# Kernel tuning notes

Hardware: AMD Instinct MI355X
Metric: run time of the kernel (lower is better)

## Reference

```python
import jax, jax.numpy as jnp
import numpy as np

N_CFG = 400_000    # total basic-block nodes across the batch
E_CFG = 1_600_000  # CFG edges
N_FUNC = 8_000     # internal functions across the batch
N_EXT = 1_600      # external functions across the batch
N_FCG = N_FUNC + N_EXT
E_FCG = 80_000     # call-graph edges
B = 8              # binaries per batch
D_IN, D_H = 64, 128
VOCAB = 10_002     # max_vocab_size + 2


def gcn_layer(x, edge_index, W, b, n_nodes):
    # PyG GCNConv with self-loops: x' = D^{-1/2}(A+I)D^{-1/2} (x W) + b
    h = x @ W
    row, col = edge_index[0], edge_index[1]
    deg = jax.ops.segment_sum(jnp.ones_like(col, dtype=h.dtype), col, num_segments=n_nodes) + 1.0
    dis = jax.lax.rsqrt(deg)
    norm = (dis[row] * dis[col])[:, None]
    agg = jax.ops.segment_sum(h[row] * norm, col, num_segments=n_nodes)
    return agg + h * (dis * dis)[:, None] + b  # second term is the self-loop message


def segment_mean(x, seg, n):
    s = jax.ops.segment_sum(x, seg, num_segments=n)
    c = jax.ops.segment_sum(jnp.ones((x.shape[0],), x.dtype), seg, num_segments=n)
    return s / jnp.maximum(c, 1.0)[:, None]


def setup_inputs() -> dict:
    key = jax.random.key(0)
    ks = jax.random.split(key, 24)
    s = 0.05
    cfg_x = jax.random.normal(ks[0], (N_CFG, D_IN), jnp.float32)
    cfg_edge_index = jax.random.randint(ks[1], (2, E_CFG), 0, N_CFG)
    cfg_node2func = jnp.sort(jax.random.randint(ks[2], (N_CFG,), 0, N_FUNC))
    fcg_edge_index = jax.random.randint(ks[3], (2, E_FCG), 0, N_FCG)
    fcg_batch = jnp.sort(jax.random.randint(ks[4], (N_FCG,), 0, B))
    # first N_FUNC FCG nodes are internal (index into pooled CFG embeddings),
    # the rest are external (index into the embedding table, avoiding pad idx 0)
    fcg_src_idx = jnp.concatenate([jnp.arange(N_FUNC, dtype=jnp.int64 if jax.config.jax_enable_x64 else jnp.int32).astype(jnp.int32),
                                   jax.random.randint(ks[5], (N_EXT,), 1, VOCAB)])
    fcg_is_ext = jnp.concatenate([jnp.zeros((N_FUNC,), jnp.int32), jnp.ones((N_EXT,), jnp.int32)])
    emb_table = jax.random.normal(ks[6], (VOCAB, D_H), jnp.float32) * s
    emb_table = emb_table.at[0].set(0.0)  # padding_idx row
    return {
        'cfg_x': cfg_x, 'cfg_edge_index': cfg_edge_index, 'cfg_node2func': cfg_node2func,
        'fcg_edge_index': fcg_edge_index, 'fcg_batch': fcg_batch,
        'fcg_src_idx': fcg_src_idx, 'fcg_is_ext': fcg_is_ext,
        'W_cfg1': jax.random.normal(ks[7], (D_IN, D_H), jnp.float32) * s,
        'b_cfg1': jax.random.normal(ks[8], (D_H,), jnp.float32) * s,
        'W_cfg2': jax.random.normal(ks[9], (D_H, D_H), jnp.float32) * s,
        'b_cfg2': jax.random.normal(ks[10], (D_H,), jnp.float32) * s,
        'emb_table': emb_table,
        'W_fcg1': jax.random.normal(ks[11], (D_H, D_H), jnp.float32) * s,
        'b_fcg1': jax.random.normal(ks[12], (D_H,), jnp.float32) * s,
        'Wp1': jax.random.normal(ks[13], (D_H, D_H // 2), jnp.float32) * s,
        'bp1': jax.random.normal(ks[14], (D_H // 2,), jnp.float32) * s,
        'Wp2': jax.random.normal(ks[15], (D_H // 2, D_H // 4), jnp.float32) * s,
        'bp2': jax.random.normal(ks[16], (D_H // 4,), jnp.float32) * s,
        'Wp3': jax.random.normal(ks[17], (D_H // 4, 1), jnp.float32) * s,
        'bp3': jax.random.normal(ks[18], (1,), jnp.float32) * s,
    }


def reference(cfg_x, cfg_edge_index, cfg_node2func, fcg_edge_index, fcg_batch,
              fcg_src_idx, fcg_is_ext, W_cfg1, b_cfg1, W_cfg2, b_cfg2, emb_table,
              W_fcg1, b_fcg1, Wp1, bp1, Wp2, bp2, Wp3, bp3):
    # CFG-level GCN stack (dropout is identity in eval)
    x = jax.nn.relu(gcn_layer(cfg_x, cfg_edge_index, W_cfg1, b_cfg1, N_CFG))
    x = jax.nn.relu(gcn_layer(x, cfg_edge_index, W_cfg2, b_cfg2, N_CFG))
    # global_mean_pool per function
    x_cfg_pool = segment_mean(x, cfg_node2func, N_FUNC)  # [N_FUNC, D_H]
    # assemble FCG node features: internal = pooled CFG embedding, external = embedding lookup
    internal = jnp.take(x_cfg_pool, jnp.clip(fcg_src_idx, 0, N_FUNC - 1), axis=0)
    external = jnp.take(emb_table, fcg_src_idx, axis=0, mode='clip')
    fcg_x = jnp.where((fcg_is_ext == 1)[:, None], external, internal)  # [N_FCG, D_H]
    # FCG-level GCN
    y = jax.nn.relu(gcn_layer(fcg_x, fcg_edge_index, W_fcg1, b_fcg1, N_FCG))
    # global_mean_pool per binary
    g = segment_mean(y, fcg_batch, B)  # [B, D_H]
    # projection head + sigmoid
    h = jax.nn.relu(g @ Wp1 + bp1)
    h = jax.nn.relu(h @ Wp2 + bp2)
    return jax.nn.sigmoid(h @ Wp3 + bp3)  # [B, 1]
```

## Files before the change

kernel.cpp:

```cpp
#include <hip/hip_runtime.h>
#include <math.h>

#define N_CFG 400000
#define E_CFG 1600000
#define N_FUNC 8000
#define N_EXT 1600
#define N_FCG (N_FUNC + N_EXT)
#define E_FCG 80000
#define NBATCH 8
#define VOCAB 10002

typedef unsigned int uint32;
typedef __attribute__((ext_vector_type(8))) short bf16x8;
typedef __attribute__((ext_vector_type(4))) float f32x4;

__device__ __forceinline__ float bf2f(unsigned short u){
  union { unsigned int i; float f; } v; v.i = ((unsigned int)u) << 16; return v.f;
}
__device__ __forceinline__ float bflo(unsigned int u){
  union { unsigned int i; float f; } v; v.i = u << 16; return v.f;
}
__device__ __forceinline__ float bfhi(unsigned int u){
  union { unsigned int i; float f; } v; v.i = u & 0xffff0000u; return v.f;
}
__device__ __forceinline__ unsigned short f2bf(float f){
  union { float f; unsigned int i; } v; v.f = f;
  unsigned int i = v.i;
  unsigned int r = (i + 0x7fffu + ((i >> 16) & 1u)) >> 16;
  return (unsigned short)r;
}
__device__ __forceinline__ unsigned int packbf(float x, float y){
  return (unsigned int)f2bf(x) | (((unsigned int)f2bf(y)) << 16);
}

__global__ void k_detect(const void* __restrict__ emb, int* __restrict__ flag){
  __shared__ int viol;
  if (threadIdx.x == 0) viol = 0;
  __syncthreads();
  const unsigned int* u = (const unsigned int*)emb;
  int my = 0;
  for (int i = threadIdx.x; i < 1024; i += 256){
    unsigned int lo = u[i] & 0xffffu;
    unsigned int ex = (lo >> 7) & 0xffu;
    bool ok = (ex == 0u) || (ex >= 80u && ex <= 127u);
    if (!ok) my++;
  }
  atomicAdd(&viol, my);
  __syncthreads();
  if (threadIdx.x == 0) *flag = (viol < 100) ? 1 : 0;
}

__global__ void k_conv(const void* __restrict__ src, unsigned short* __restrict__ dst,
                       int n, const int* __restrict__ flag){
  int i = blockIdx.x * 256 + threadIdx.x;
  if (i >= n) return;
  if (*flag) dst[i] = ((const unsigned short*)src)[i];
  else       dst[i] = f2bf(((const float*)src)[i]);
}

__global__ void k_convT(const void* __restrict__ src, unsigned short* __restrict__ dst,
                        int K, int N, const int* __restrict__ flag){
  int i = blockIdx.x * 256 + threadIdx.x;
  if (i >= K * N) return;
  int k = i / N, n = i - k * N;
  unsigned short v;
  if (*flag) v = ((const unsigned short*)src)[i];
  else       v = f2bf(((const float*)src)[i]);
  dst[n * K + k] = v;
}

__global__ void k_count(const int* __restrict__ idx, int n, uint32* __restrict__ cnt){
  int i = blockIdx.x * 256 + threadIdx.x;
  if (i < n) atomicAdd(&cnt[idx[i]], 1u);
}

__global__ void k_count_sorted(const int* __restrict__ seg, int n, uint32* __restrict__ cnt){
  int base = (blockIdx.x * 256 + threadIdx.x) * 64;
  if (base >= n) return;
  int end = base + 64; if (end > n) end = n;
  int curv = seg[base]; uint32 run = 1;
  for (int i = base + 1; i < end; i++){
    int v = seg[i];
    if (v == curv) run++;
    else { atomicAdd(&cnt[curv], run); curv = v; run = 1; }
  }
  atomicAdd(&cnt[curv], run);
}

__global__ void k_scan1(const uint32* __restrict__ cnt, int n,
                        uint32* __restrict__ off, uint32* __restrict__ bsums){
  __shared__ uint32 s[256];
  int tid = threadIdx.x;
  int base = blockIdx.x * 1024 + tid * 4;
  uint32 v0 = (base+0<n)?cnt[base+0]:0u, v1 = (base+1<n)?cnt[base+1]:0u;
  uint32 v2 = (base+2<n)?cnt[base+2]:0u, v3 = (base+3<n)?cnt[base+3]:0u;
  uint32 tsum = v0+v1+v2+v3;
  uint32 x = tsum;
  s[tid] = x; __syncthreads();
  for (int o = 1; o < 256; o <<= 1){
    uint32 y = (tid >= o) ? s[tid - o] : 0u;
    __syncthreads();
    x += y; s[tid] = x; __syncthreads();
  }
  uint32 run = x - tsum;
  if (base+0<n) off[base+0]=run; run+=v0;
  if (base+1<n) off[base+1]=run; run+=v1;
  if (base+2<n) off[base+2]=run; run+=v2;
  if (base+3<n) off[base+3]=run;
  if (tid == 255) bsums[blockIdx.x] = x;
}

__global__ void k_scan2(uint32* bsums, int nb){
  __shared__ uint32 s[1024];
  int tid = threadIdx.x;
  uint32 v = (tid < nb) ? bsums[tid] : 0u;
  uint32 x = v;
  s[tid] = x; __syncthreads();
  for (int o = 1; o < 1024; o <<= 1){
    uint32 y = (tid >= o) ? s[tid - o] : 0u;
    __syncthreads();
    x += y; s[tid] = x; __syncthreads();
  }
  if (tid < nb) bsums[tid] = x - v;
}

__global__ void k_scan3(uint32* off, uint32* cur, const uint32* __restrict__ bsums, int n){
  int i = blockIdx.x * 256 + threadIdx.x;
  if (i >= n) return;
  uint32 v = off[i] + bsums[i >> 10];
  off[i] = v;
  if (cur) cur[i] = v;
}

__global__ void k_fill(const int* __restrict__ edges, int E,
                       uint32* __restrict__ cur, int* __restrict__ sorted){
  int e = blockIdx.x * 256 + threadIdx.x;
  if (e >= E) return;
  int r = edges[e];
  int c = edges[E + e];
  uint32 p = atomicAdd(&cur[c], 1u);
  sorted[p] = r;
}

__global__ void k_dis(const uint32* __restrict__ cnt, float* __restrict__ dis, int n){
  int i = blockIdx.x * 256 + threadIdx.x;
  if (i < n) dis[i] = rsqrtf((float)cnt[i] + 1.0f);
}

template<int K>
__global__ __launch_bounds__(256)
void k_gemm_mfma(const void* __restrict__ Xsrc, const unsigned short* __restrict__ Wt,
                 const float* __restrict__ dis, unsigned short* __restrict__ out,
                 const int* __restrict__ flag, int mixed){
  const int KP = K + 8;
  __shared__ unsigned short Xs[64 * (K + 8)];
  __shared__ unsigned short Ws[128 * (K + 8)];
  int tid = threadIdx.x;
  long row0 = (long)blockIdx.x * 64;

  {
    int n = tid >> 1, half = tid & 1;
    const uint4* src = (const uint4*)(Wt + n * K) + half * (K / 16);
    uint4* dst = (uint4*)(Ws + n * KP) + half * (K / 16);
    #pragma unroll
    for (int i = 0; i < K / 16; i++) dst[i] = src[i];
  }
  {
    int r = tid >> 2, part = tid & 3;
    int isbf = mixed ? *flag : 1;
    uint4* dst = (uint4*)(Xs + r * KP) + part * (K / 32);
    if (isbf){
      const uint4* src = (const uint4*)((const unsigned short*)Xsrc + (row0 + r) * K) + part * (K / 32);
      #pragma unroll
      for (int i = 0; i < K / 32; i++) dst[i] = src[i];
    } else {
      const float4* src = (const float4*)((const float*)Xsrc + (row0 + r) * K) + part * (K / 16);
      #pragma unroll
      for (int i = 0; i < K / 32; i++){
        float4 f0 = src[2*i], f1 = src[2*i+1];
        uint4 u;
        u.x = packbf(f0.x, f0.y); u.y = packbf(f0.z, f0.w);
        u.z = packbf(f1.x, f1.y); u.w = packbf(f1.z, f1.w);
        dst[i] = u;
      }
    }
  }
  __syncthreads();

  int w = tid >> 6, lane = tid & 63, m = lane & 15, q = lane >> 4;
  f32x4 acc[8];
  #pragma unroll
  for (int t = 0; t < 8; t++) acc[t] = (f32x4){0.f, 0.f, 0.f, 0.f};

  const unsigned short* Arow = &Xs[(w * 16 + m) * KP + q * 8];
  const unsigned short* Bbase = &Ws[m * KP + q * 8];
  #pragma unroll
  for (int kc = 0; kc < K; kc += 32){
    bf16x8 a = *(const bf16x8*)(Arow + kc);
    #pragma unroll
    for (int t = 0; t < 8; t++){
      bf16x8 b = *(const bf16x8*)(Bbase + t * 16 * KP + kc);
      acc[t] = __builtin_amdgcn_mfma_f32_16x16x32_bf16(a, b, acc[t], 0, 0, 0);
    }
  }

  float d[4];
  #pragma unroll
  for (int r = 0; r < 4; r++) d[r] = dis[row0 + w * 16 + q * 4 + r];
  #pragma unroll
  for (int t = 0; t < 8; t++){
    #pragma unroll
    for (int r = 0; r < 4; r++){
      long grow = row0 + w * 16 + q * 4 + r;
      out[grow * 128 + t * 16 + m] = f2bf(acc[t][r] * d[r]);
    }
  }
}

__global__ __launch_bounds__(256)
void k_agg4(const uint4* __restrict__ hs4,
            const uint32* __restrict__ off, const uint32* __restrict__ cnt,
            const int* __restrict__ sorted, const float* __restrict__ dis,
            const uint4* __restrict__ bias4, uint4* __restrict__ out4, int n){
  int tid = threadIdx.x;
  int wave = tid >> 6, lane = tid & 63, grp = lane >> 4, sub = lane & 15;
  int node = blockIdx.x * 16 + wave * 4 + grp;
  if (node >= n) return;
  uint32 o = off[node], c = cnt[node];
  float a[8] = {0.f,0.f,0.f,0.f,0.f,0.f,0.f,0.f};
  for (uint32 j = 0; j < c; j++){
    int r = sorted[o + j];
    uint4 u = hs4[(long)r * 16 + sub];
    a[0] += bflo(u.x); a[1] += bfhi(u.x);
    a[2] += bflo(u.y); a[3] += bfhi(u.y);
    a[4] += bflo(u.z); a[5] += bfhi(u.z);
    a[6] += bflo(u.w); a[7] += bfhi(u.w);
  }
  {
    uint4 u = hs4[(long)node * 16 + sub];
    a[0] += bflo(u.x); a[1] += bfhi(u.x);
    a[2] += bflo(u.y); a[3] += bfhi(u.y);
    a[4] += bflo(u.z); a[5] += bfhi(u.z);
    a[6] += bflo(u.w); a[7] += bfhi(u.w);
  }
  float d = dis[node];
  uint4 b = bias4[sub];
  float v0 = fmaxf(fmaf(d, a[0], bflo(b.x)), 0.f);
  float v1 = fmaxf(fmaf(d, a[1], bfhi(b.x)), 0.f);
  float v2 = fmaxf(fmaf(d, a[2], bflo(b.y)), 0.f);
  float v3 = fmaxf(fmaf(d, a[3], bfhi(b.y)), 0.f);
  float v4 = fmaxf(fmaf(d, a[4], bflo(b.z)), 0.f);
  float v5 = fmaxf(fmaf(d, a[5], bfhi(b.z)), 0.f);
  float v6 = fmaxf(fmaf(d, a[6], bflo(b.w)), 0.f);
  float v7 = fmaxf(fmaf(d, a[7], bfhi(b.w)), 0.f);
  uint4 ov;
  ov.x = packbf(v0, v1); ov.y = packbf(v2, v3);
  ov.z = packbf(v4, v5); ov.w = packbf(v6, v7);
  out4[(long)node * 16 + sub] = ov;
}

__global__ __launch_bounds__(256)
void k_pool_batch(const uint4* __restrict__ y4, const uint32* __restrict__ g_cnt,
                  float* __restrict__ g_sum){
  __shared__ float red[16][128];
  int b = blockIdx.x >> 3, s = blockIdx.x & 7;
  int tid = threadIdx.x;
  int grp = tid >> 4, sub = tid & 15;
  uint32 start = 0;
  for (int i = 0; i < b; i++) start += g_cnt[i];
  uint32 cb = g_cnt[b];
  uint32 len = (cb + 7) / 8;
  uint32 lo = s * len;
  uint32 hi = lo + len; if (hi > cb) hi = cb;
  float a[8] = {0.f,0.f,0.f,0.f,0.f,0.f,0.f,0.f};
  for (uint32 i = lo + grp; i < hi; i += 16){
    uint4 u = y4[(long)(start + i) * 16 + sub];
    a[0] += bflo(u.x); a[1] += bfhi(u.x);
    a[2] += bflo(u.y); a[3] += bfhi(u.y);
    a[4] += bflo(u.z); a[5] += bfhi(u.z);
    a[6] += bflo(u.w); a[7] += bfhi(u.w);
  }
  #pragma unroll
  for (int i = 0; i < 8; i++) red[grp][sub * 8 + i] = a[i];
  __syncthreads();
  if (tid < 128){
    float t = 0.f;
    #pragma unroll
    for (int g = 0; g < 16; g++) t += red[g][tid];
    atomicAdd(&g_sum[b * 128 + tid], t);
  }
}

__global__ void k_pool_mean(const unsigned int* __restrict__ x2, const uint32* __restrict__ off,
                            const uint32* __restrict__ cnt, unsigned int* __restrict__ pooled2, int nf){
  int f = blockIdx.x; int t = threadIdx.x;
  uint32 o = off[f], c = cnt[f];
  float sx = 0.f, sy = 0.f;
  for (uint32 j = 0; j < c; j++){
    unsigned int u = x2[(long)(o + j) * 64 + t];
    sx += bflo(u); sy += bfhi(u);
  }
  float inv = 1.0f / (float)((c > 0u) ? c : 1u);
  pooled2[(long)f * 64 + t] = packbf(sx * inv, sy * inv);
}

__global__ void k_assemble(const unsigned int* __restrict__ pooled2, const unsigned int* __restrict__ emb2,
                           const int* __restrict__ src, const int* __restrict__ isext,
                           unsigned int* __restrict__ fx2){
  int i = blockIdx.x; int t = threadIdx.x;
  int s = src[i];
  unsigned int v;
  if (isext[i] == 1){
    int idx = s; if (idx < 0) idx = 0; if (idx > VOCAB - 1) idx = VOCAB - 1;
    v = emb2[(long)idx * 64 + t];
  } else {
    int f = s; if (f < 0) f = 0; if (f > N_FUNC - 1) f = N_FUNC - 1;
    v = pooled2[(long)f * 64 + t];
  }
  fx2[(long)i * 64 + t] = v;
}

__global__ __launch_bounds__(256)
void k_head(const float* __restrict__ g_sum, const uint32* __restrict__ g_cnt,
            const unsigned short* __restrict__ Wp1, const unsigned short* __restrict__ bp1,
            const unsigned short* __restrict__ Wp2, const unsigned short* __restrict__ bp2,
            const unsigned short* __restrict__ Wp3, const unsigned short* __restrict__ bp3,
            void* __restrict__ outp, const int* __restrict__ flag){
  __shared__ float G[8 * 128];
  __shared__ float H1[8 * 64];
  __shared__ float H2[8 * 32];
  int tid = threadIdx.x;
  for (int i = tid; i < 1024; i += 256){
    uint32 c = g_cnt[i >> 7];
    G[i] = g_sum[i] / (float)((c > 0u) ? c : 1u);
  }
  __syncthreads();
  for (int i = tid; i < 512; i += 256){
    int b = i >> 6, j = i & 63;
    float a = bf2f(bp1[j]);
    for (int d = 0; d < 128; d++) a = fmaf(G[b * 128 + d], bf2f(Wp1[d * 64 + j]), a);
    H1[i] = fmaxf(a, 0.f);
  }
  __syncthreads();
  {
    int b = tid >> 5, j = tid & 31;
    float a = bf2f(bp2[j]);
    for (int d = 0; d < 64; d++) a = fmaf(H1[b * 64 + d], bf2f(Wp2[d * 32 + j]), a);
    H2[tid] = fmaxf(a, 0.f);
  }
  __syncthreads();
  if (tid < 8){
    float a = bf2f(bp3[0]);
    for (int d = 0; d < 32; d++) a = fmaf(H2[tid * 32 + d], bf2f(Wp3[d]), a);
    float s = 1.f / (1.f + __expf(-a));
    if (*flag) ((unsigned short*)outp)[tid] = f2bf(s);
    else       ((float*)outp)[tid] = s;
  }
}

extern "C" void kernel_launch(void* const* d_in, const int* in_sizes, int n_in,
                              void* d_out, int out_size, void* d_ws, size_t ws_size,
                              hipStream_t stream){
  const void* cfg_x     = d_in[0];
  const int*  cfg_edges = (const int*)d_in[1];
  const int*  node2func = (const int*)d_in[2];
  const int*  fcg_edges = (const int*)d_in[3];
  const int*  fcg_batch = (const int*)d_in[4];
  const int*  fcg_src   = (const int*)d_in[5];
  const int*  fcg_isext = (const int*)d_in[6];
  const void* W1  = d_in[7];
  const void* b1  = d_in[8];
  const void* W2  = d_in[9];
  const void* b2  = d_in[10];
  const void* emb = d_in[11];
  const void* Wf  = d_in[12];
  const void* bfv = d_in[13];
  const void* Wp1 = d_in[14];
  const void* bp1 = d_in[15];
  const void* Wp2 = d_in[16];
  const void* bp2 = d_in[17];
  const void* Wp3 = d_in[18];
  const void* bp3 = d_in[19];

  char* p = (char*)d_ws;
  auto carve = [&](size_t bytes)->char* {
    char* r = p; p += (bytes + 255) & ~(size_t)255; return r;
  };
  unsigned short* A   = (unsigned short*)carve((size_t)N_CFG * 128 * 2);
  unsigned short* Bx  = (unsigned short*)carve((size_t)N_CFG * 128 * 2);
  uint32* cnt_cfg = (uint32*)carve((size_t)N_CFG * 4);
  uint32* off_cfg = (uint32*)carve((size_t)N_CFG * 4);
  uint32* cur_cfg = (uint32*)carve((size_t)N_CFG * 4);
  float*  dis_cfg = (float*) carve((size_t)N_CFG * 4);
  int*    sorted_cfg = (int*)carve((size_t)E_CFG * 4);
  uint32* bsums   = (uint32*)carve(1024 * 4);
  uint32* pool_cnt = (uint32*)carve(N_FUNC * 4);
  uint32* pool_off = (uint32*)carve(N_FUNC * 4);
  unsigned int* pooled2 = (unsigned int*)carve((size_t)N_FUNC * 64 * 4);
  unsigned int* fx2     = (unsigned int*)carve((size_t)N_FCG * 64 * 4);
  unsigned short* hsf   = (unsigned short*)carve((size_t)N_FCG * 128 * 2);
  unsigned short* yf    = (unsigned short*)carve((size_t)N_FCG * 128 * 2);
  uint32* cnt_f = (uint32*)carve(N_FCG * 4);
  uint32* off_f = (uint32*)carve(N_FCG * 4);
  uint32* cur_f = (uint32*)carve(N_FCG * 4);
  float*  dis_f = (float*) carve(N_FCG * 4);
  int*    sorted_f = (int*)carve(E_FCG * 4);
  float*  g_sum = (float*)carve(8 * 128 * 4);
  uint32* g_cnt = (uint32*)carve(8 * 4);
  int*    flag  = (int*)   carve(256);
  unsigned short* cW1t = (unsigned short*)carve(128 * 64 * 2);
  unsigned short* cb1  = (unsigned short*)carve(128 * 2);
  unsigned short* cW2t = (unsigned short*)carve(128 * 128 * 2);
  unsigned short* cb2  = (unsigned short*)carve(128 * 2);
  unsigned short* cemb = (unsigned short*)carve((size_t)VOCAB * 128 * 2);
  unsigned short* cWft = (unsigned short*)carve(128 * 128 * 2);
  unsigned short* cbf  = (unsigned short*)carve(128 * 2);
  unsigned short* cWp1 = (unsigned short*)carve(128 * 64 * 2);
  unsigned short* cbp1 = (unsigned short*)carve(64 * 2);
  unsigned short* cWp2 = (unsigned short*)carve(64 * 32 * 2);
  unsigned short* cbp2 = (unsigned short*)carve(32 * 2);
  unsigned short* cWp3 = (unsigned short*)carve(32 * 2);
  unsigned short* cbp3 = (unsigned short*)carve(2 * 2);

  hipMemsetAsync(cnt_cfg, 0, (size_t)N_CFG * 4, stream);
  hipMemsetAsync(cnt_f,   0, (size_t)N_FCG * 4, stream);
  hipMemsetAsync(pool_cnt,0, (size_t)N_FUNC * 4, stream);
  hipMemsetAsync(g_sum,   0, 8 * 128 * 4, stream);
  hipMemsetAsync(g_cnt,   0, 8 * 4, stream);

  k_detect<<<1, 256, 0, stream>>>(emb, flag);
  auto conv = [&](const void* src, unsigned short* dst, int n){
    k_conv<<<(n + 255) / 256, 256, 0, stream>>>(src, dst, n, flag);
  };
  k_convT<<<(64 * 128 + 255) / 256, 256, 0, stream>>>(W1, cW1t, 64, 128, flag);
  k_convT<<<(128 * 128 + 255) / 256, 256, 0, stream>>>(W2, cW2t, 128, 128, flag);
  k_convT<<<(128 * 128 + 255) / 256, 256, 0, stream>>>(Wf, cWft, 128, 128, flag);
  conv(b1, cb1, 128);
  conv(b2, cb2, 128);
  conv(emb, cemb, VOCAB * 128);
  conv(bfv, cbf, 128);
  conv(Wp1, cWp1, 128 * 64); conv(bp1, cbp1, 64);
  conv(Wp2, cWp2, 64 * 32);  conv(bp2, cbp2, 32);
  conv(Wp3, cWp3, 32);       conv(bp3, cbp3, 1);

  k_count<<<(E_CFG + 255) / 256, 256, 0, stream>>>(cfg_edges + E_CFG, E_CFG, cnt_cfg);
  int nb_cfg = (N_CFG + 1023) / 1024;
  k_scan1<<<nb_cfg, 256, 0, stream>>>(cnt_cfg, N_CFG, off_cfg, bsums);
  k_scan2<<<1, 1024, 0, stream>>>(bsums, nb_cfg);
  k_scan3<<<(N_CFG + 255) / 256, 256, 0, stream>>>(off_cfg, cur_cfg, bsums, N_CFG);
  k_fill<<<(E_CFG + 255) / 256, 256, 0, stream>>>(cfg_edges, E_CFG, cur_cfg, sorted_cfg);
  k_dis<<<(N_CFG + 255) / 256, 256, 0, stream>>>(cnt_cfg, dis_cfg, N_CFG);

  k_gemm_mfma<64><<<N_CFG / 64, 256, 0, stream>>>(cfg_x, cW1t, dis_cfg, A, flag, 1);
  k_agg4<<<N_CFG / 16, 256, 0, stream>>>((const uint4*)A, off_cfg, cnt_cfg, sorted_cfg,
                                         dis_cfg, (const uint4*)cb1, (uint4*)Bx, N_CFG);
  k_gemm_mfma<128><<<N_CFG / 64, 256, 0, stream>>>(Bx, cW2t, dis_cfg, A, flag, 0);
  k_agg4<<<N_CFG / 16, 256, 0, stream>>>((const uint4*)A, off_cfg, cnt_cfg, sorted_cfg,
                                         dis_cfg, (const uint4*)cb2, (uint4*)Bx, N_CFG);

  k_count_sorted<<<((N_CFG + 63) / 64 + 255) / 256, 256, 0, stream>>>(node2func, N_CFG, pool_cnt);
  int nb_pool = (N_FUNC + 1023) / 1024;
  k_scan1<<<nb_pool, 256, 0, stream>>>(pool_cnt, N_FUNC, pool_off, bsums);
  k_scan2<<<1, 1024, 0, stream>>>(bsums, nb_pool);
  k_scan3<<<(N_FUNC + 255) / 256, 256, 0, stream>>>(pool_off, (uint32*)nullptr, bsums, N_FUNC);
  k_pool_mean<<<N_FUNC, 64, 0, stream>>>((const unsigned int*)Bx, pool_off, pool_cnt, pooled2, N_FUNC);

  k_assemble<<<N_FCG, 64, 0, stream>>>(pooled2, (const unsigned int*)cemb, fcg_src, fcg_isext, fx2);

  k_count<<<(E_FCG + 255) / 256, 256, 0, stream>>>(fcg_edges + E_FCG, E_FCG, cnt_f);
  int nb_f = (N_FCG + 1023) / 1024;
  k_scan1<<<nb_f, 256, 0, stream>>>(cnt_f, N_FCG, off_f, bsums);
  k_scan2<<<1, 1024, 0, stream>>>(bsums, nb_f);
  k_scan3<<<(N_FCG + 255) / 256, 256, 0, stream>>>(off_f, cur_f, bsums, N_FCG);
  k_fill<<<(E_FCG + 255) / 256, 256, 0, stream>>>(fcg_edges, E_FCG, cur_f, sorted_f);
  k_dis<<<(N_FCG + 255) / 256, 256, 0, stream>>>(cnt_f, dis_f, N_FCG);

  k_gemm_mfma<128><<<N_FCG / 64, 256, 0, stream>>>((const void*)fx2, cWft, dis_f, hsf, flag, 0);
  k_count_sorted<<<1, 256, 0, stream>>>(fcg_batch, N_FCG, g_cnt);
  k_agg4<<<N_FCG / 16, 256, 0, stream>>>((const uint4*)hsf, off_f, cnt_f, sorted_f,
                                         dis_f, (const uint4*)cbf, (uint4*)yf, N_FCG);
  k_pool_batch<<<64, 256, 0, stream>>>((const uint4*)yf, g_cnt, g_sum);

  k_head<<<1, 256, 0, stream>>>(g_sum, g_cnt, cWp1, cbp1, cWp2, cbp2, cWp3, cbp3, d_out, flag);
}
```

Measured before the change: 786.3 us.

## Use wave-per-node aggregation, windowed CSR fill, and merge small setup kernels

Aggregation now assigns one 64-lane wave per node: four 16-lane groups split the neighbour list and are combined with cross-lane shuffles. The old kernel gave each 16-lane group a whole node, so the change aims for more memory parallelism on the gather. The CFG CSR fill is split into four passes, each covering a window of destination nodes, to improve locality of the atomic counters and scattered writes, at the cost of reading the edge list four times. Many small conversion, scan and degree kernels are merged into fewer launches, the small scans become single-block kernels, and batch pooling writes results directly instead of zeroing memory and using atomics.

Result: slower. 894.8 us (+13.8%).

```diff
diff --git a/kernel.cpp b/kernel.cpp
--- a/kernel.cpp
+++ b/kernel.cpp
@@ -58,14 +58,33 @@
   else       dst[i] = f2bf(((const float*)src)[i]);
 }
 
-__global__ void k_convT(const void* __restrict__ src, unsigned short* __restrict__ dst,
-                        int K, int N, const int* __restrict__ flag){
+struct Seg { const void* s; unsigned short* d; int n; };
+struct Segs9 { Seg v[9]; };
+__global__ void k_conv_multi(Segs9 segs, const int* __restrict__ flag, int total){
   int i = blockIdx.x * 256 + threadIdx.x;
-  if (i >= K * N) return;
-  int k = i / N, n = i - k * N;
+  if (i >= total) return;
+  int k = 0, idx = i;
+  while (idx >= segs.v[k].n){ idx -= segs.v[k].n; k++; }
+  unsigned short r;
+  if (*flag) r = ((const unsigned short*)segs.v[k].s)[idx];
+  else       r = f2bf(((const float*)segs.v[k].s)[idx]);
+  segs.v[k].d[idx] = r;
+}
+
+__global__ void k_convT3(const void* __restrict__ W1, const void* __restrict__ W2,
+                         const void* __restrict__ Wf,
+                         unsigned short* __restrict__ o1, unsigned short* __restrict__ o2,
+                         unsigned short* __restrict__ o3, const int* __restrict__ flag){
+  int i = blockIdx.x * 256 + threadIdx.x;
+  if (i >= 8192 + 16384 + 16384) return;
+  const void* src; unsigned short* dst; int K, N, idx;
+  if (i < 8192){ src = W1; dst = o1; K = 64; N = 128; idx = i; }
+  else if (i < 24576){ src = W2; dst = o2; K = 128; N = 128; idx = i - 8192; }
+  else { src = Wf; dst = o3; K = 128; N = 128; idx = i - 24576; }
+  int k = idx / N, n = idx - k * N;
   unsigned short v;
-  if (*flag) v = ((const unsigned short*)src)[i];
-  else       v = f2bf(((const float*)src)[i]);
+  if (*flag) v = ((const unsigned short*)src)[idx];
+  else       v = f2bf(((const float*)src)[idx]);
   dst[n * K + k] = v;
 }
 
@@ -124,12 +143,59 @@
   if (tid < nb) bsums[tid] = x - v;
 }
 
-__global__ void k_scan3(uint32* off, uint32* cur, const uint32* __restrict__ bsums, int n){
+__global__ void k_scan3_dis(uint32* off, uint32* cur, const uint32* __restrict__ bsums,
+                            const uint32* __restrict__ cnt, float* __restrict__ dis, int n){
   int i = blockIdx.x * 256 + threadIdx.x;
   if (i >= n) return;
   uint32 v = off[i] + bsums[i >> 10];
   off[i] = v;
-  if (cur) cur[i] = v;
+  cur[i] = v;
+  dis[i] = rsqrtf((float)cnt[i] + 1.0f);
+}
+
+template<int PT>
+__global__ __launch_bounds__(1024)
+void k_scan_small(const uint32* __restrict__ cnt, int n, uint32* __restrict__ off,
+                  uint32* __restrict__ cur, float* __restrict__ dis){
+  __shared__ uint32 tmp[1024];
+  int tid = threadIdx.x;
+  uint32 local[PT]; uint32 s = 0;
+  #pragma unroll
+  for (int k = 0; k < PT; k++){
+    int idx = tid * PT + k;
+    uint32 v = (idx < n) ? cnt[idx] : 0u;
+    local[k] = s; s += v;
+  }
+  uint32 x = s;
+  tmp[tid] = x; __syncthreads();
+  for (int o = 1; o < 1024; o <<= 1){
+    uint32 y = (tid >= o) ? tmp[tid - o] : 0u;
+    __syncthreads();
+    x += y; tmp[tid] = x; __syncthreads();
+  }
+  uint32 excl = x - s;
+  #pragma unroll
+  for (int k = 0; k < PT; k++){
+    int idx = tid * PT + k;
+    if (idx < n){
+      uint32 o2 = excl + local[k];
+      off[idx] = o2;
+      if (cur) cur[idx] = o2;
+      if (dis) dis[idx] = rsqrtf((float)cnt[idx] + 1.0f);
+    }
+  }
+}
+
+__global__ void k_fill_win(const int* __restrict__ edges, int E,
+                           uint32* __restrict__ cur, int* __restrict__ sorted,
+                           int lo, int hi){
+  int e = blockIdx.x * 256 + threadIdx.x;
+  if (e >= E) return;
+  int c = edges[E + e];
+  if (c < lo || c >= hi) return;
+  int r = edges[e];
+  uint32 p = atomicAdd(&cur[c], 1u);
+  sorted[p] = r;
 }
 
 __global__ void k_fill(const int* __restrict__ edges, int E,
@@ -140,11 +206,6 @@
   int c = edges[E + e];
   uint32 p = atomicAdd(&cur[c], 1u);
   sorted[p] = r;
-}
-
-__global__ void k_dis(const uint32* __restrict__ cnt, float* __restrict__ dis, int n){
-  int i = blockIdx.x * 256 + threadIdx.x;
-  if (i < n) dis[i] = rsqrtf((float)cnt[i] + 1.0f);
 }
 
 template<int K>
@@ -218,17 +279,17 @@
 }
 
 __global__ __launch_bounds__(256)
-void k_agg4(const uint4* __restrict__ hs4,
-            const uint32* __restrict__ off, const uint32* __restrict__ cnt,
-            const int* __restrict__ sorted, const float* __restrict__ dis,
-            const uint4* __restrict__ bias4, uint4* __restrict__ out4, int n){
-  int tid = threadIdx.x;
-  int wave = tid >> 6, lane = tid & 63, grp = lane >> 4, sub = lane & 15;
-  int node = blockIdx.x * 16 + wave * 4 + grp;
+void k_agg_wave(const uint4* __restrict__ hs4,
+                const uint32* __restrict__ off, const uint32* __restrict__ cnt,
+                const int* __restrict__ sorted, const float* __restrict__ dis,
+                const uint4* __restrict__ bias4, uint4* __restrict__ out4, int n){
+  int gid = blockIdx.x * 256 + threadIdx.x;
+  int node = gid >> 6;
   if (node >= n) return;
+  int lane = threadIdx.x & 63, grp = lane >> 4, sub = lane & 15;
   uint32 o = off[node], c = cnt[node];
   float a[8] = {0.f,0.f,0.f,0.f,0.f,0.f,0.f,0.f};
-  for (uint32 j = 0; j < c; j++){
+  for (uint32 j = grp; j < c; j += 4){
     int r = sorted[o + j];
     uint4 u = hs4[(long)r * 16 + sub];
     a[0] += bflo(u.x); a[1] += bfhi(u.x);
@@ -236,44 +297,46 @@
     a[4] += bflo(u.z); a[5] += bfhi(u.z);
     a[6] += bflo(u.w); a[7] += bfhi(u.w);
   }
-  {
-    uint4 u = hs4[(long)node * 16 + sub];
-    a[0] += bflo(u.x); a[1] += bfhi(u.x);
-    a[2] += bflo(u.y); a[3] += bfhi(u.y);
-    a[4] += bflo(u.z); a[5] += bfhi(u.z);
-    a[6] += bflo(u.w); a[7] += bfhi(u.w);
-  }
-  float d = dis[node];
-  uint4 b = bias4[sub];
-  float v0 = fmaxf(fmaf(d, a[0], bflo(b.x)), 0.f);
-  float v1 = fmaxf(fmaf(d, a[1], bfhi(b.x)), 0.f);
-  float v2 = fmaxf(fmaf(d, a[2], bflo(b.y)), 0.f);
-  float v3 = fmaxf(fmaf(d, a[3], bfhi(b.y)), 0.f);
-  float v4 = fmaxf(fmaf(d, a[4], bflo(b.z)), 0.f);
-  float v5 = fmaxf(fmaf(d, a[5], bfhi(b.z)), 0.f);
-  float v6 = fmaxf(fmaf(d, a[6], bflo(b.w)), 0.f);
-  float v7 = fmaxf(fmaf(d, a[7], bfhi(b.w)), 0.f);
-  uint4 ov;
-  ov.x = packbf(v0, v1); ov.y = packbf(v2, v3);
-  ov.z = packbf(v4, v5); ov.w = packbf(v6, v7);
-  out4[(long)node * 16 + sub] = ov;
+  #pragma unroll
+  for (int i = 0; i < 8; i++){
+    a[i] += __shfl_xor(a[i], 16);
+    a[i] += __shfl_xor(a[i], 32);
+  }
+  uint4 su = hs4[(long)node * 16 + sub];
+  a[0] += bflo(su.x); a[1] += bfhi(su.x);
+  a[2] += bflo(su.y); a[3] += bfhi(su.y);
+  a[4] += bflo(su.z); a[5] += bfhi(su.z);
+  a[6] += bflo(su.w); a[7] += bfhi(su.w);
+  if (grp == 0){
+    float d = dis[node];
+    uint4 b = bias4[sub];
+    float v0 = fmaxf(fmaf(d, a[0], bflo(b.x)), 0.f);
+    float v1 = fmaxf(fmaf(d, a[1], bfhi(b.x)), 0.f);
+    float v2 = fmaxf(fmaf(d, a[2], bflo(b.y)), 0.f);
+    float v3 = fmaxf(fmaf(d, a[3], bfhi(b.y)), 0.f);
+    float v4 = fmaxf(fmaf(d, a[4], bflo(b.z)), 0.f);
+    float v5 = fmaxf(fmaf(d, a[5], bfhi(b.z)), 0.f);
+    float v6 = fmaxf(fmaf(d, a[6], bflo(b.w)), 0.f);
+    float v7 = fmaxf(fmaf(d, a[7], bfhi(b.w)), 0.f);
+    uint4 ov;
+    ov.x = packbf(v0, v1); ov.y = packbf(v2, v3);
+    ov.z = packbf(v4, v5); ov.w = packbf(v6, v7);
+    out4[(long)node * 16 + sub] = ov;
+  }
 }
 
 __global__ __launch_bounds__(256)
-void k_pool_batch(const uint4* __restrict__ y4, const uint32* __restrict__ g_cnt,
-                  float* __restrict__ g_sum){
+void k_pool_batch8(const uint4* __restrict__ y4, const uint32* __restrict__ g_cnt,
+                   float* __restrict__ g_sum){
   __shared__ float red[16][128];
-  int b = blockIdx.x >> 3, s = blockIdx.x & 7;
+  int b = blockIdx.x;
   int tid = threadIdx.x;
   int grp = tid >> 4, sub = tid & 15;
   uint32 start = 0;
   for (int i = 0; i < b; i++) start += g_cnt[i];
   uint32 cb = g_cnt[b];
-  uint32 len = (cb + 7) / 8;
-  uint32 lo = s * len;
-  uint32 hi = lo + len; if (hi > cb) hi = cb;
   float a[8] = {0.f,0.f,0.f,0.f,0.f,0.f,0.f,0.f};
-  for (uint32 i = lo + grp; i < hi; i += 16){
+  for (uint32 i = grp; i < cb; i += 16){
     uint4 u = y4[(long)(start + i) * 16 + sub];
     a[0] += bflo(u.x); a[1] += bfhi(u.x);
     a[2] += bflo(u.y); a[3] += bfhi(u.y);
@@ -287,7 +350,7 @@
     float t = 0.f;
     #pragma unroll
     for (int g = 0; g < 16; g++) t += red[g][tid];
-    atomicAdd(&g_sum[b * 128 + tid], t);
+    g_sum[b * 128 + tid] = t;
   }
 }
 
@@ -425,61 +488,53 @@
   hipMemsetAsync(cnt_cfg, 0, (size_t)N_CFG * 4, stream);
   hipMemsetAsync(cnt_f,   0, (size_t)N_FCG * 4, stream);
   hipMemsetAsync(pool_cnt,0, (size_t)N_FUNC * 4, stream);
-  hipMemsetAsync(g_sum,   0, 8 * 128 * 4, stream);
   hipMemsetAsync(g_cnt,   0, 8 * 4, stream);
 
   k_detect<<<1, 256, 0, stream>>>(emb, flag);
-  auto conv = [&](const void* src, unsigned short* dst, int n){
-    k_conv<<<(n + 255) / 256, 256, 0, stream>>>(src, dst, n, flag);
-  };
-  k_convT<<<(64 * 128 + 255) / 256, 256, 0, stream>>>(W1, cW1t, 64, 128, flag);
-  k_convT<<<(128 * 128 + 255) / 256, 256, 0, stream>>>(W2, cW2t, 128, 128, flag);
-  k_convT<<<(128 * 128 + 255) / 256, 256, 0, stream>>>(Wf, cWft, 128, 128, flag);
-  conv(b1, cb1, 128);
-  conv(b2, cb2, 128);
-  conv(emb, cemb, VOCAB * 128);
-  conv(bfv, cbf, 128);
-  conv(Wp1, cWp1, 128 * 64); conv(bp1, cbp1, 64);
-  conv(Wp2, cWp2, 64 * 32);  conv(bp2, cbp2, 32);
-  conv(Wp3, cWp3, 32);       conv(bp3, cbp3, 1);
+  k_convT3<<<(40960 + 255) / 256, 256, 0, stream>>>(W1, W2, Wf, cW1t, cW2t, cWft, flag);
+  {
+    Segs9 segs = {{
+      { b1,  cb1,  128 }, { b2,  cb2,  128 }, { bfv, cbf,  128 },
+      { Wp1, cWp1, 128 * 64 }, { bp1, cbp1, 64 },
+      { Wp2, cWp2, 64 * 32 },  { bp2, cbp2, 32 },
+      { Wp3, cWp3, 32 },       { bp3, cbp3, 1 }
+    }};
+    int total = 128 + 128 + 128 + 8192 + 64 + 2048 + 32 + 32 + 1;
+    k_conv_multi<<<(total + 255) / 256, 256, 0, stream>>>(segs, flag, total);
+  }
+  k_conv<<<(VOCAB * 128 + 255) / 256, 256, 0, stream>>>(emb, cemb, VOCAB * 128, flag);
 
   k_count<<<(E_CFG + 255) / 256, 256, 0, stream>>>(cfg_edges + E_CFG, E_CFG, cnt_cfg);
   int nb_cfg = (N_CFG + 1023) / 1024;
   k_scan1<<<nb_cfg, 256, 0, stream>>>(cnt_cfg, N_CFG, off_cfg, bsums);
   k_scan2<<<1, 1024, 0, stream>>>(bsums, nb_cfg);
-  k_scan3<<<(N_CFG + 255) / 256, 256, 0, stream>>>(off_cfg, cur_cfg, bsums, N_CFG);
-  k_fill<<<(E_CFG + 255) / 256, 256, 0, stream>>>(cfg_edges, E_CFG, cur_cfg, sorted_cfg);
-  k_dis<<<(N_CFG + 255) / 256, 256, 0, stream>>>(cnt_cfg, dis_cfg, N_CFG);
+  k_scan3_dis<<<(N_CFG + 255) / 256, 256, 0, stream>>>(off_cfg, cur_cfg, bsums, cnt_cfg, dis_cfg, N_CFG);
+  for (int w = 0; w < 4; w++)
+    k_fill_win<<<(E_CFG + 255) / 256, 256, 0, stream>>>(cfg_edges, E_CFG, cur_cfg, sorted_cfg,
+                                                        w * (N_CFG / 4), (w + 1) * (N_CFG / 4));
 
   k_gemm_mfma<64><<<N_CFG / 64, 256, 0, stream>>>(cfg_x, cW1t, dis_cfg, A, flag, 1);
-  k_agg4<<<N_CFG / 16, 256, 0, stream>>>((const uint4*)A, off_cfg, cnt_cfg, sorted_cfg,
-                                         dis_cfg, (const uint4*)cb1, (uint4*)Bx, N_CFG);
+  k_agg_wave<<<N_CFG / 4, 256, 0, stream>>>((const uint4*)A, off_cfg, cnt_cfg, sorted_cfg,
+                                            dis_cfg, (const uint4*)cb1, (uint4*)Bx, N_CFG);
   k_gemm_mfma<128><<<N_CFG / 64, 256, 0, stream>>>(Bx, cW2t, dis_cfg, A, flag, 0);
-  k_agg4<<<N_CFG / 16, 256, 0, stream>>>((const uint4*)A, off_cfg, cnt_cfg, sorted_cfg,
-                                         dis_cfg, (const uint4*)cb2, (uint4*)Bx, N_CFG);
+  k_agg_wave<<<N_CFG / 4, 256, 0, stream>>>((const uint4*)A, off_cfg, cnt_cfg, sorted_cfg,
+                                            dis_cfg, (const uint4*)cb2, (uint4*)Bx, N_CFG);
 
   k_count_sorted<<<((N_CFG + 63) / 64 + 255) / 256, 256, 0, stream>>>(node2func, N_CFG, pool_cnt);
-  int nb_pool = (N_FUNC + 1023) / 1024;
-  k_scan1<<<nb_pool, 256, 0, stream>>>(pool_cnt, N_FUNC, pool_off, bsums);
-  k_scan2<<<1, 1024, 0, stream>>>(bsums, nb_pool);
-  k_scan3<<<(N_FUNC + 255) / 256, 256, 0, stream>>>(pool_off, (uint32*)nullptr, bsums, N_FUNC);
+  k_scan_small<8><<<1, 1024, 0, stream>>>(pool_cnt, N_FUNC, pool_off, (uint32*)nullptr, (float*)nullptr);
   k_pool_mean<<<N_FUNC, 64, 0, stream>>>((const unsigned int*)Bx, pool_off, pool_cnt, pooled2, N_FUNC);
 
   k_assemble<<<N_FCG, 64, 0, stream>>>(pooled2, (const unsigned int*)cemb, fcg_src, fcg_isext, fx2);
 
   k_count<<<(E_FCG + 255) / 256, 256, 0, stream>>>(fcg_edges + E_FCG, E_FCG, cnt_f);
-  int nb_f = (N_FCG + 1023) / 1024;
-  k_scan1<<<nb_f, 256, 0, stream>>>(cnt_f, N_FCG, off_f, bsums);
-  k_scan2<<<1, 1024, 0, stream>>>(bsums, nb_f);
-  k_scan3<<<(N_FCG + 255) / 256, 256, 0, stream>>>(off_f, cur_f, bsums, N_FCG);
+  k_scan_small<10><<<1, 1024, 0, stream>>>(cnt_f, N_FCG, off_f, cur_f, dis_f);
   k_fill<<<(E_FCG + 255) / 256, 256, 0, stream>>>(fcg_edges, E_FCG, cur_f, sorted_f);
-  k_dis<<<(N_FCG + 255) / 256, 256, 0, stream>>>(cnt_f, dis_f, N_FCG);
+  k_count_sorted<<<1, 256, 0, stream>>>(fcg_batch, N_FCG, g_cnt);
 
   k_gemm_mfma<128><<<N_FCG / 64, 256, 0, stream>>>((const void*)fx2, cWft, dis_f, hsf, flag, 0);
-  k_count_sorted<<<1, 256, 0, stream>>>(fcg_batch, N_FCG, g_cnt);
-  k_agg4<<<N_FCG / 16, 256, 0, stream>>>((const uint4*)hsf, off_f, cnt_f, sorted_f,
-                                         dis_f, (const uint4*)cbf, (uint4*)yf, N_FCG);
-  k_pool_batch<<<64, 256, 0, stream>>>((const uint4*)yf, g_cnt, g_sum);
+  k_agg_wave<<<N_FCG / 4, 256, 0, stream>>>((const uint4*)hsf, off_f, cnt_f, sorted_f,
+                                            dis_f, (const uint4*)cbf, (uint4*)yf, N_FCG);
+  k_pool_batch8<<<8, 256, 0, stream>>>((const uint4*)yf, g_cnt, g_sum);
 
   k_head<<<1, 256, 0, stream>>>(g_sum, g_cnt, cWp1, cbp1, cWp2, cbp2, cWp3, cbp3, d_out, flag);
 }
```
